# Performance work log

Measured on AMD Instinct MI355X. Metric: run time of the kernel, lower is better.

## Reference

```python
import jax, jax.numpy as jnp
import numpy as np

DIM_IN = 1024
DIM_OUT = 1024
CTX = 2048


def setup_inputs() -> dict:
    key = jax.random.key(0)
    k_x, k_q, k_k, k_v = jax.random.split(key, 4)
    x = jax.random.normal(k_x, (4, CTX, DIM_IN), dtype=jnp.float32)
    # nn.Linear default init ~ U(-1/sqrt(fan_in), 1/sqrt(fan_in)); scale doesn't matter for correctness
    s = 1.0 / np.sqrt(DIM_IN)
    Wq = jax.random.uniform(k_q, (DIM_IN, DIM_OUT), jnp.float32, -s, s)
    Wk = jax.random.uniform(k_k, (DIM_IN, DIM_OUT), jnp.float32, -s, s)
    Wv = jax.random.uniform(k_v, (DIM_IN, DIM_OUT), jnp.float32, -s, s)
    return {"x": x, "Wq": Wq, "Wk": Wk, "Wv": Wv}


def reference(x, Wq, Wk, Wv):
    # x: [B, T, D_in]; W*: [D_in, D_out]
    b, t, _ = x.shape
    q = jnp.einsum('btd,de->bte', x, Wq)
    k = jnp.einsum('btd,de,->bte', x, Wk, jnp.float32(1.0)) if False else jnp.einsum('btd,de->bte', x, Wk)
    v = jnp.einsum('btd,de->bte', x, Wv)
    scores = jnp.einsum('bqe,bke->bqk', q, k)  # [B, T, T]
    causal = jnp.tril(jnp.ones((t, t), dtype=bool))  # True where allowed
    scores = jnp.where(causal, scores, -jnp.inf)
    weights = jax.nn.softmax(scores / jnp.sqrt(jnp.float32(k.shape[-1])), axis=-1)
    # dropout p=0.0 -> identity
    return jnp.einsum('bqk,bke->bqe', weights, v)
```

## Files before the change

### kernel.cpp

```cpp
#include <hip/hip_runtime.h>


using f32x4 = __attribute__((ext_vector_type(4))) float;
using s16x8 = __attribute__((ext_vector_type(8))) short;

#define CTX 2048
#define DIM 1024
#define NB 4

__device__ __forceinline__ short f2bf(float f) {
  union { float f; unsigned u; } v; v.f = f;
  unsigned r = (v.u + 0x7fffu + ((v.u >> 16) & 1u)) >> 16;
  return (short)r;
}

__device__ __forceinline__ void async16(const void* g, void* l) {
  __builtin_amdgcn_global_load_lds(
      (const __attribute__((address_space(1))) void*)g,
      (__attribute__((address_space(3))) void*)l, 16, 0, 0);
}


__global__ __launch_bounds__(256) void cvt_x(const float* __restrict__ in,
                                             short* __restrict__ out, long n8) {
  long i = (long)blockIdx.x * 256 + threadIdx.x;
  if (i >= n8) return;
  const float4* p = (const float4*)in;
  float4 a = p[i * 2], b = p[i * 2 + 1];
  short o[8];
  o[0] = f2bf(a.x); o[1] = f2bf(a.y); o[2] = f2bf(a.z); o[3] = f2bf(a.w);
  o[4] = f2bf(b.x); o[5] = f2bf(b.y); o[6] = f2bf(b.z); o[7] = f2bf(b.w);
  *(int4*)&out[i * 8] = *(int4*)o;
}

__global__ __launch_bounds__(256) void cvt_wT(const float* __restrict__ Wq,
                                              const float* __restrict__ Wk,
                                              const float* __restrict__ Wv,
                                              short* __restrict__ WT) {
  int z = blockIdx.z;
  const float* W = (z == 0) ? Wq : (z == 1) ? Wk : Wv;
  short* o = WT + (long)z * DIM * DIM;
  __shared__ float t[32][33];
  int n0 = blockIdx.x * 32, k0 = blockIdx.y * 32;
  int tx = threadIdx.x, ty = threadIdx.y;
  #pragma unroll
  for (int j = 0; j < 4; ++j)
    t[ty + j * 8][tx] = W[(long)(k0 + ty + j * 8) * DIM + n0 + tx];
  __syncthreads();
  #pragma unroll
  for (int j = 0; j < 4; ++j)
    o[(long)(n0 + ty + j * 8) * DIM + k0 + tx] = f2bf(t[tx][ty + j * 8]);
}

template <int MODE, bool CSKIP, bool KLIM>
__global__ __launch_bounds__(256) void gemm_bt(const short* __restrict__ A,
                                               const short* __restrict__ B,
                                               void* __restrict__ Cout,
                                               int M, int N, int K,
                                               long sA, long sB, long sC, int ldc) {
  const int bx = blockIdx.x, by = blockIdx.y, bz = blockIdx.z;
  if (CSKIP && by > bx) return;
  const short* Ab = A + bz * sA + (long)bx * 128 * K;
  const short* Bb = B + bz * sB + (long)by * 128 * K;
  __shared__ short As[128 * 32];
  __shared__ short Bs[128 * 32];
  const int tid = threadIdx.x;
  const int lane = tid & 63, wid = tid >> 6;
  const int wr = wid >> 1, wc = wid & 1;
  const int frow = lane & 15, kgrp = lane >> 4;

  f32x4 acc[4][4];
  const f32x4 zero = {0.f, 0.f, 0.f, 0.f};
  #pragma unroll
  for (int m = 0; m < 4; ++m)
    #pragma unroll
    for (int n = 0; n < 4; ++n) acc[m][n] = zero;

  int kt_end = K >> 5;
  if (KLIM) { int lim = (bx + 1) << 2; if (lim < kt_end) kt_end = lim; }

  const int e0 = wid * 512 + lane * 8;

  for (int kt = 0; kt < kt_end; ++kt) {
    const int k0 = kt << 5;
    __syncthreads();
    #pragma unroll
    for (int p = 0; p < 2; ++p) {
      const int e = e0 + (p << 11);
      const int r = e >> 5, c = e & 31;
      async16(Ab + (long)r * K + (k0 + c), &As[e]);
      async16(Bb + (long)r * K + (k0 + c), &Bs[e]);
    }
    __syncthreads();

    s16x8 af[4], bfr[4];
    #pragma unroll
    for (int m = 0; m < 4; ++m)
      af[m] = *(const s16x8*)&As[((wr << 6) + (m << 4) + frow) * 32 + (kgrp << 3)];
    #pragma unroll
    for (int n = 0; n < 4; ++n)
      bfr[n] = *(const s16x8*)&Bs[((wc << 6) + (n << 4) + frow) * 32 + (kgrp << 3)];
    #pragma unroll
    for (int m = 0; m < 4; ++m)
      #pragma unroll
      for (int n = 0; n < 4; ++n)
        acc[m][n] = __builtin_amdgcn_mfma_f32_16x16x32_bf16(af[m], bfr[n], acc[m][n], 0, 0, 0);
  }

  const int row0 = (bx << 7) + (wr << 6);
  const int col0 = (by << 7) + (wc << 6);
  #pragma unroll
  for (int m = 0; m < 4; ++m) {
    #pragma unroll
    for (int n = 0; n < 4; ++n) {
      #pragma unroll
      for (int r = 0; r < 4; ++r) {
        const int row = row0 + (m << 4) + (kgrp << 2) + r;
        const int col = col0 + (n << 4) + frow;
        const float v = acc[m][n][r];
        if (MODE == 0) {
          ((short*)Cout)[bz * sC + (long)row * ldc + col] = f2bf(v);
        } else if (MODE == 1) {
          const long off = (long)(row >> 11) * ((long)N * CTX) + (long)col * CTX + (row & (CTX - 1));
          ((short*)Cout)[off] = f2bf(v);
        } else if (MODE == 2) {
          ((_Float16*)Cout)[bz * sC + (long)row * ldc + col] = (_Float16)v;
        } else {
          ((float*)Cout)[bz * sC + (long)row * ldc + col] = v;
        }
      }
    }
  }
}

__global__ __launch_bounds__(256) void softmax_causal(void* __restrict__ Sbuf) {
  const int r = blockIdx.x, b = blockIdx.y;
  const long base = (long)b * CTX * CTX + (long)r * CTX;
  _Float16* S = (_Float16*)Sbuf + base;
  short* P = (short*)Sbuf + base;
  const int tid = threadIdx.x;
  const int lane = tid & 63, wid = tid >> 6;
  const int c0 = tid * 8;
  const float scale = 0.03125f;

  _Float16 h[8];
  *(int4*)h = *(const int4*)&S[c0];
  float v[8];
  float m = -INFINITY;
  #pragma unroll
  for (int j = 0; j < 8; ++j) {
    v[j] = (c0 + j <= r) ? (float)h[j] * scale : -INFINITY;
    m = fmaxf(m, v[j]);
  }
  #pragma unroll
  for (int off = 32; off >= 1; off >>= 1) m = fmaxf(m, __shfl_xor(m, off));
  __shared__ float redm[4], reds[4];
  if (lane == 0) redm[wid] = m;
  __syncthreads();
  m = fmaxf(fmaxf(redm[0], redm[1]), fmaxf(redm[2], redm[3]));

  float p[8];
  float s = 0.f;
  #pragma unroll
  for (int j = 0; j < 8; ++j) {
    p[j] = exp2f((v[j] - m) * 1.44269504f);
    s += p[j];
  }
  #pragma unroll
  for (int off = 32; off >= 1; off >>= 1) s += __shfl_xor(s, off);
  if (lane == 0) reds[wid] = s;
  __syncthreads();
  s = reds[0] + reds[1] + reds[2] + reds[3];
  const float inv = 1.0f / s;

  short o[8];
  #pragma unroll
  for (int j = 0; j < 8; ++j) o[j] = f2bf(p[j] * inv);
  *(int4*)&P[c0] = *(int4*)o;
}

extern "C" void kernel_launch(void* const* d_in, const int* in_sizes, int n_in,
                              void* d_out, int out_size, void* d_ws, size_t ws_size,
                              hipStream_t stream) {
  (void)in_sizes; (void)n_in; (void)out_size; (void)ws_size;
  const float* x  = (const float*)d_in[0];
  const float* Wq = (const float*)d_in[1];
  const float* Wk = (const float*)d_in[2];
  const float* Wv = (const float*)d_in[3];

  const long MB = 1024 * 1024;
  char* ws = (char*)d_ws;
  short* xb = (short*)(ws + 0);
  short* WT = (short*)(ws + 16 * MB);
  short* Qb = (short*)(ws + 24 * MB);
  short* Kb = (short*)(ws + 40 * MB);
  short* Vt = (short*)(ws + 56 * MB);
  void*  S  = (void*)(ws + 72 * MB);

  cvt_x<<<4096, 256, 0, stream>>>(x, xb, (long)NB * CTX * DIM / 8);
  cvt_wT<<<dim3(32, 32, 3), dim3(32, 8), 0, stream>>>(Wq, Wk, Wv, WT);
  gemm_bt<0, false, false><<<dim3(64, 8, 2), 256, 0, stream>>>(
      xb, WT, Qb, NB * CTX, DIM, DIM, 0, (long)DIM * DIM, (long)NB * CTX * DIM, DIM);
  gemm_bt<1, false, false><<<dim3(64, 8, 1), 256, 0, stream>>>(
      xb, WT + 2L * DIM * DIM, Vt, NB * CTX, DIM, DIM, 0, 0, 0, DIM);
  gemm_bt<2, true, false><<<dim3(16, 16, NB), 256, 0, stream>>>(
      Qb, Kb, S, CTX, CTX, DIM, (long)CTX * DIM, (long)CTX * DIM, (long)CTX * CTX, CTX);
  softmax_causal<<<dim3(CTX, NB), 256, 0, stream>>>(S);
  gemm_bt<3, false, true><<<dim3(16, 8, NB), 256, 0, stream>>>(
      (short*)S, Vt, d_out, CTX, DIM, CTX, (long)CTX * CTX, (long)DIM * CTX, (long)CTX * DIM, DIM);
}
```

Measured before the change: 312.3 us.

## Double-buffer GEMM LDS tiles and fuse QKV projections into one launch

The GEMM main loop now double-buffers its shared-memory tiles. The async global-to-LDS loads for the next k-tile are issued before the MFMAs on the current tile, with one wait and barrier per iteration instead of two. This overlaps load latency with compute at the cost of twice the LDS per block. The Q/K and V projection GEMMs are merged into a single launch over a 3*DIM-wide N. The epilogue routes columns to Q, K, or the transposed V layout, which removes one launch and lets all three projections share a wave of blocks.

```diff
diff --git a/kernel.cpp b/kernel.cpp
--- a/kernel.cpp
+++ b/kernel.cpp
@@ -62,8 +62,8 @@
   if (CSKIP && by > bx) return;
   const short* Ab = A + bz * sA + (long)bx * 128 * K;
   const short* Bb = B + bz * sB + (long)by * 128 * K;
-  __shared__ short As[128 * 32];
-  __shared__ short Bs[128 * 32];
+  __shared__ short As[2][128 * 32];
+  __shared__ short Bs[2][128 * 32];
   const int tid = threadIdx.x;
   const int lane = tid & 63, wid = tid >> 6;
   const int wr = wid >> 1, wc = wid & 1;
@@ -80,31 +80,47 @@
   if (KLIM) { int lim = (bx + 1) << 2; if (lim < kt_end) kt_end = lim; }
 
   const int e0 = wid * 512 + lane * 8;
-
+  const int er = e0 >> 5, ec = e0 & 31;
+
+  #pragma unroll
+  for (int p = 0; p < 2; ++p) {
+    const int e = e0 + (p << 11);
+    const int r = er + (p << 6);
+    async16(Ab + (long)r * K + ec, &As[0][e]);
+    async16(Bb + (long)r * K + ec, &Bs[0][e]);
+  }
+  asm volatile("s_waitcnt vmcnt(0)");
+  __syncthreads();
+
+  int cur = 0;
   for (int kt = 0; kt < kt_end; ++kt) {
-    const int k0 = kt << 5;
-    __syncthreads();
-    #pragma unroll
-    for (int p = 0; p < 2; ++p) {
-      const int e = e0 + (p << 11);
-      const int r = e >> 5, c = e & 31;
-      async16(Ab + (long)r * K + (k0 + c), &As[e]);
-      async16(Bb + (long)r * K + (k0 + c), &Bs[e]);
+    if (kt + 1 < kt_end) {
+      const int k0n = (kt + 1) << 5;
+      #pragma unroll
+      for (int p = 0; p < 2; ++p) {
+        const int e = e0 + (p << 11);
+        const int r = er + (p << 6);
+        async16(Ab + (long)r * K + (k0n + ec), &As[cur ^ 1][e]);
+        async16(Bb + (long)r * K + (k0n + ec), &Bs[cur ^ 1][e]);
+      }
     }
-    __syncthreads();
 
     s16x8 af[4], bfr[4];
     #pragma unroll
     for (int m = 0; m < 4; ++m)
-      af[m] = *(const s16x8*)&As[((wr << 6) + (m << 4) + frow) * 32 + (kgrp << 3)];
+      af[m] = *(const s16x8*)&As[cur][((wr << 6) + (m << 4) + frow) * 32 + (kgrp << 3)];
     #pragma unroll
     for (int n = 0; n < 4; ++n)
-      bfr[n] = *(const s16x8*)&Bs[((wc << 6) + (n << 4) + frow) * 32 + (kgrp << 3)];
+      bfr[n] = *(const s16x8*)&Bs[cur][((wc << 6) + (n << 4) + frow) * 32 + (kgrp << 3)];
     #pragma unroll
     for (int m = 0; m < 4; ++m)
       #pragma unroll
       for (int n = 0; n < 4; ++n)
         acc[m][n] = __builtin_amdgcn_mfma_f32_16x16x32_bf16(af[m], bfr[n], acc[m][n], 0, 0, 0);
+
+    asm volatile("s_waitcnt vmcnt(0)");
+    __syncthreads();
+    cur ^= 1;
   }
 
   const int row0 = (bx << 7) + (wr << 6);
@@ -118,15 +134,20 @@
         const int row = row0 + (m << 4) + (kgrp << 2) + r;
         const int col = col0 + (n << 4) + frow;
         const float v = acc[m][n][r];
-        if (MODE == 0) {
-          ((short*)Cout)[bz * sC + (long)row * ldc + col] = f2bf(v);
-        } else if (MODE == 1) {
-          const long off = (long)(row >> 11) * ((long)N * CTX) + (long)col * CTX + (row & (CTX - 1));
+        if (MODE == 2) {
+          ((_Float16*)Cout)[bz * sC + (long)row * ldc + col] = (_Float16)v;
+        } else if (MODE == 3) {
+          ((float*)Cout)[bz * sC + (long)row * ldc + col] = v;
+        } else {
+          const long QK = (long)NB * CTX * DIM;
+          long off;
+          if (col < 2048) {
+            off = (long)(col >> 10) * QK + (long)row * DIM + (col & 1023);
+          } else {
+            off = 2 * QK + (long)(row >> 11) * ((long)DIM * CTX) +
+                  (long)(col - 2048) * CTX + (row & (CTX - 1));
+          }
           ((short*)Cout)[off] = f2bf(v);
-        } else if (MODE == 2) {
-          ((_Float16*)Cout)[bz * sC + (long)row * ldc + col] = (_Float16)v;
-        } else {
-          ((float*)Cout)[bz * sC + (long)row * ldc + col] = v;
         }
       }
     }
@@ -199,10 +220,8 @@
 
   cvt_x<<<4096, 256, 0, stream>>>(x, xb, (long)NB * CTX * DIM / 8);
   cvt_wT<<<dim3(32, 32, 3), dim3(32, 8), 0, stream>>>(Wq, Wk, Wv, WT);
-  gemm_bt<0, false, false><<<dim3(64, 8, 2), 256, 0, stream>>>(
-      xb, WT, Qb, NB * CTX, DIM, DIM, 0, (long)DIM * DIM, (long)NB * CTX * DIM, DIM);
-  gemm_bt<1, false, false><<<dim3(64, 8, 1), 256, 0, stream>>>(
-      xb, WT + 2L * DIM * DIM, Vt, NB * CTX, DIM, DIM, 0, 0, 0, DIM);
+  gemm_bt<4, false, false><<<dim3(64, 24, 1), 256, 0, stream>>>(
+      xb, WT, Qb, NB * CTX, 3 * DIM, DIM, 0, 0, 0, DIM);
   gemm_bt<2, true, false><<<dim3(16, 16, NB), 256, 0, stream>>>(
       Qb, Kb, S, CTX, CTX, DIM, (long)CTX * DIM, (long)CTX * DIM, (long)CTX * CTX, CTX);
   softmax_causal<<<dim3(CTX, NB), 256, 0, stream>>>(S);
```

Result: faster. 285.0 us (-8.8%).
